# Kernel tuning notes

Measured on AMD Instinct MI355X. Metric: run time of the kernel, lower is better.

Reference implementation:

```python
import jax, jax.numpy as jnp
import numpy as np

H = 16  # heads
EPS_LN = 1e-5

def _ln(x, g, b):
    m = jnp.mean(x, axis=-1, keepdims=True)
    v = jnp.mean((x - m) ** 2, axis=-1, keepdims=True)
    return (x - m) / jnp.sqrt(v + EPS_LN) * g + b

def setup_inputs() -> dict:
    key = jax.random.key(0)
    B, L, d, mlp = 4, 4096, 1024, 4096
    ks = jax.random.split(key, 12)
    s = 0.02
    inp = {
        'x':   jax.random.normal(ks[0], (B, L, d), jnp.float32),
        'Wq':  jax.random.normal(ks[1], (d, d), jnp.float32) * s,
        'bq':  jnp.zeros((d,), jnp.float32),
        'gq':  jnp.ones((d,), jnp.float32),
        'betaq': jnp.zeros((d,), jnp.float32),
        'Wk':  jax.random.normal(ks[2], (d, d), jnp.float32) * s,
        'bk':  jnp.zeros((d,), jnp.float32),
        'gk':  jnp.ones((d,), jnp.float32),
        'betak': jnp.zeros((d,), jnp.float32),
        'Wv':  jax.random.normal(ks[3], (d, d), jnp.float32) * s,
        'bv':  jnp.zeros((d,), jnp.float32),
        'gv':  jnp.ones((d,), jnp.float32),
        'betav': jnp.zeros((d,), jnp.float32),
        'Wfq': jax.random.normal(ks[4], (d, d), jnp.float32) * s,
        'bfq': jnp.zeros((d,), jnp.float32),
        'Wfk': jax.random.normal(ks[5], (d, d), jnp.float32) * s,
        'bfk': jnp.zeros((d,), jnp.float32),
        'ga':  jnp.ones((d,), jnp.float32),
        'ba':  jnp.zeros((d,), jnp.float32),
        'W1':  jax.random.normal(ks[6], (d, mlp), jnp.float32) * s,
        'b1':  jnp.zeros((mlp,), jnp.float32),
        'W2':  jax.random.normal(ks[7], (mlp, d), jnp.float32) * s,
        'b2':  jnp.zeros((d,), jnp.float32),
    }
    return inp

def _fwd(x, Wq, bq, gq, betaq, Wk, bk, gk, betak, Wv, bv, gv, betav,
         Wfq, bfq, Wfk, bfk, ga, ba, W1, b1, W2, b2):
    B, L, d = x.shape
    D = d // H
    # Q/K/V projections + LayerNorm (dropout is eval-mode identity)
    Q = _ln(x @ Wq + bq, gq, betaq)                      # [B,L,d]
    Kc = _ln(x @ Wk + bk, gk, betak)                     # [B,L,d]
    Vc = _ln(x @ Wv + bv, gv, betav)                     # [B,L,d]
    # prepend zero token to K and V (add_zero_token=True)
    z = jnp.zeros((B, 1, d), x.dtype)
    K = jnp.concatenate([z, Kc], axis=1)                 # [B,Lk,d], Lk=L+1
    V = jnp.concatenate([z, Vc], axis=1)
    # kernel feature maps: tanh(Linear(.)) + 1
    phi_Q = jnp.tanh(Q @ Wfq + bfq) + 1.0
    phi_K = jnp.tanh(K @ Wfk + bfk) + 1.0
    split = lambda t: t.reshape(B, t.shape[1], H, D).transpose(0, 2, 1, 3)
    Qh, Kh, Vh = split(Q), split(K), split(V)            # [B,H,L(,k),D]
    pQ, pK = split(phi_Q), split(phi_K)
    # probe-softmax gating of phi_K
    q_probe = jnp.mean(Qh, axis=2) / jnp.sqrt(jnp.asarray(D, x.dtype))  # [B,H,D]
    score = jax.nn.softmax(jnp.einsum('bhd,bhkd->bhk', q_probe, Kh), axis=-1)  # [B,H,Lk]
    pKw = pK * score[..., None]                          # [B,H,Lk,D]
    # linear-attention fast path
    KV = jnp.einsum('bhkd,bhke->bhde', pKw, Vh)          # [B,H,D,D]
    Ksum = jnp.sum(pKw, axis=2)                          # [B,H,D]
    num = jnp.einsum('bhqd,bhde->bhqe', pQ, KV)          # [B,H,L,D]
    den = jnp.einsum('bhqd,bhd->bhq', pQ, Ksum)[..., None] + 1e-6
    out = num / den                                      # [B,H,L,D]
    out = out.transpose(0, 2, 1, 3).reshape(B, L, d)     # merge heads
    a = _ln(out, ga, ba)                                 # attn_norm
    # Residual MLP: a + Linear2(GELU(Linear1(a)))  (exact erf GELU)
    h = a + (jax.nn.gelu(a @ W1 + b1, approximate=False) @ W2 + b2)
    return h + x                                         # outer residual

def reference(x, Wq, bq, gq, betaq, Wk, bk, gk, betak, Wv, bv, gv, betav,
              Wfq, bfq, Wfk, bfk, ga, ba, W1, b1, W2, b2):
    return _fwd(x, Wq, bq, gq, betaq, Wk, bk, gk, betak, Wv, bv, gv, betav,
                Wfq, bfq, Wfk, bfk, ga, ba, W1, b1, W2, b2)
```

## Files before the change

kernel.cpp:

```cpp
#include <hip/hip_runtime.h>
#include <cstddef>
#include <cstdint>

static constexpr int Bc   = 4;
static constexpr int Lq   = 4096;
static constexpr int Dm   = 1024;
static constexpr int Dmlp = 4096;
static constexpr int Mrows = Bc * Lq;
static constexpr int Lk1   = Lq + 1;

typedef unsigned short u16;
typedef __bf16 bf16_t;
typedef bf16_t bf16x8 __attribute__((ext_vector_type(8)));
typedef float  f32x4  __attribute__((ext_vector_type(4)));

__device__ __forceinline__ u16 f2b(float f) {
    uint32_t u = __builtin_bit_cast(uint32_t, f);
    return (u16)((u + 0x7FFFu + ((u >> 16) & 1u)) >> 16);
}
__device__ __forceinline__ float b2f(u16 h) {
    uint32_t u = ((uint32_t)h) << 16;
    return __builtin_bit_cast(float, u);
}

#define GLL16(gsrc, ldst) \
    __builtin_amdgcn_global_load_lds( \
        (const __attribute__((address_space(1))) void*)(gsrc), \
        (__attribute__((address_space(3))) void*)(ldst), 16, 0, 0)

__global__ __launch_bounds__(256)
void zero_kernel(float* __restrict__ p, int n) {
    const int i = blockIdx.x * 256 + threadIdx.x;
    if (i < n) p[i] = 0.0f;
}

__global__ __launch_bounds__(256)
void cvt_bf16_kernel(const float* __restrict__ in, u16* __restrict__ outp, int n) {
    for (int i = (blockIdx.x * 256 + threadIdx.x) * 4; i < n; i += gridDim.x * 256 * 4) {
        float4 v = *(const float4*)&in[i];
        ushort4 o = { f2b(v.x), f2b(v.y), f2b(v.z), f2b(v.w) };
        *(ushort4*)&outp[i] = o;
    }
}

__global__ __launch_bounds__(256)
void transpose_bf16_kernel(const float* __restrict__ in, u16* __restrict__ outp,
                           int R, int C) {
    __shared__ float tile[64][65];
    const int r0 = blockIdx.y * 64, c0 = blockIdx.x * 64;
    const int t = threadIdx.x;
    const int lr = t >> 2, lc0 = (t & 3) * 16;
    #pragma unroll
    for (int j = 0; j < 4; ++j) {
        float4 v = *(const float4*)&in[(size_t)(r0 + lr) * C + c0 + lc0 + j * 4];
        tile[lr][lc0 + j * 4 + 0] = v.x;
        tile[lr][lc0 + j * 4 + 1] = v.y;
        tile[lr][lc0 + j * 4 + 2] = v.z;
        tile[lr][lc0 + j * 4 + 3] = v.w;
    }
    __syncthreads();
    const int oc = t >> 2, rr0 = (t & 3) * 16;
    union { u16 u[16]; uint4 v[2]; } pk;
    #pragma unroll
    for (int j = 0; j < 16; ++j) pk.u[j] = f2b(tile[rr0 + j][oc]);
    u16* po = &outp[(size_t)(c0 + oc) * R + r0 + rr0];
    *(uint4*)&po[0] = pk.v[0];
    *(uint4*)&po[8] = pk.v[1];
}

__global__ __launch_bounds__(256)
void kvt_cvt_kernel(const float* __restrict__ KV, u16* __restrict__ KVT) {
    const int bh = blockIdx.x;
    __shared__ float t[64][65];
    const int tid = threadIdx.x;
    const int r = tid >> 2, c0 = (tid & 3) * 16;
    const float* src = &KV[(size_t)bh * 4096];
    #pragma unroll
    for (int j = 0; j < 4; ++j) {
        float4 v = *(const float4*)&src[r * 64 + c0 + j * 4];
        t[r][c0 + j * 4 + 0] = v.x;
        t[r][c0 + j * 4 + 1] = v.y;
        t[r][c0 + j * 4 + 2] = v.z;
        t[r][c0 + j * 4 + 3] = v.w;
    }
    __syncthreads();
    const int e = tid >> 2, d0 = (tid & 3) * 16;
    union { u16 u[16]; uint4 v[2]; } pk;
    #pragma unroll
    for (int j = 0; j < 16; ++j) pk.u[j] = f2b(t[d0 + j][e]);
    u16* po = &KVT[(size_t)bh * 4096 + e * 64 + d0];
    *(uint4*)&po[0] = pk.v[0];
    *(uint4*)&po[8] = pk.v[1];
}

template<int ACT, bool RES, bool ACCUM, bool BIAS, bool OBF16>
__global__ __launch_bounds__(512, 1)
void mfma_gemm256(const u16* __restrict__ A, int ldA,
                  const u16* __restrict__ Bt, int ldB,
                  const float* __restrict__ bias,
                  void* __restrict__ Cout,
                  const u16* __restrict__ res1, const float* __restrict__ res2,
                  int M, int N, int K) {
    __shared__ u16 ldsA[4][8192];
    __shared__ u16 ldsB[4][8192];
    const int tid = threadIdx.x;
    const int l   = tid & 63;
    const int w   = tid >> 6;
    const int wm  = w >> 2;
    const int wn  = w & 3;
    const int l16 = l & 15, l4 = l >> 4;

    const int gx = N >> 8;
    int bid = blockIdx.x;
    bid = (bid & 7) * ((int)gridDim.x >> 3) + (bid >> 3);
    const int brow = (bid / gx) << 8;
    const int bcol = (bid % gx) << 8;

    const int srow = w * 16 + (l >> 2);
    const int skof = ((l & 3) ^ ((l >> 3) & 3)) << 3;
    const u16* gA = A  + (size_t)(brow + srow) * ldA + skof;
    const u16* gB = Bt + (size_t)(bcol + srow) * ldB + skof;
    const size_t gsA = (size_t)128 * ldA;
    const size_t gsB = (size_t)128 * ldB;
    const int ldst = w * 512 + l * 8;

    const int koff_rd = ((l4 ^ ((l16 >> 1) & 3)) << 3);
    const int aRdBase = (wm * 128 + l16) * 32 + koff_rd;
    const int bRdBase = (wn * 64  + l16) * 32 + koff_rd;

    f32x4 acc[8][4];
    const f32x4 zf = {0.f, 0.f, 0.f, 0.f};
    #pragma unroll
    for (int m = 0; m < 8; ++m)
        #pragma unroll
        for (int n = 0; n < 4; ++n) acc[m][n] = zf;

    auto stageA = [&](int slot, int kelem) {
        const u16* s = gA + (size_t)kelem;
        GLL16(s,       &ldsA[slot][ldst]);
        GLL16(s + gsA, &ldsA[slot][ldst + 4096]);
    };
    auto stageB = [&](int slot, int kelem) {
        const u16* s = gB + (size_t)kelem;
        GLL16(s,       &ldsB[slot][ldst]);
        GLL16(s + gsB, &ldsB[slot][ldst + 4096]);
    };

    const int T = K >> 5;
    stageA(0, 0);  stageB(0, 0);
    stageA(1, 32); stageB(1, 32);
    stageA(2, 64); stageB(2, 64);

    auto step = [&](int t, int waitsel, bool do_stage) {
        asm volatile("s_waitcnt lgkmcnt(0)" ::: "memory");
        if (waitsel == 0)      asm volatile("s_waitcnt vmcnt(8)" ::: "memory");
        else if (waitsel == 1) asm volatile("s_waitcnt vmcnt(4)" ::: "memory");
        else                   asm volatile("s_waitcnt vmcnt(0)" ::: "memory");
        asm volatile("s_barrier" ::: "memory");
        const int slot = t & 3;
        bf16x8 afr[4], bfr[4];
        #pragma unroll
        for (int n = 0; n < 4; ++n)
            bfr[n] = *(const bf16x8*)&ldsB[slot][bRdBase + n * 512];
        #pragma unroll
        for (int m = 0; m < 4; ++m)
            afr[m] = *(const bf16x8*)&ldsA[slot][aRdBase + m * 512];
        if (do_stage) stageA((t + 3) & 3, (t + 3) * 32);
        __builtin_amdgcn_s_setprio(1);
        #pragma unroll
        for (int m = 0; m < 4; ++m)
            #pragma unroll
            for (int n = 0; n < 4; ++n)
                acc[m][n] = __builtin_amdgcn_mfma_f32_16x16x32_bf16(
                    afr[m], bfr[n], acc[m][n], 0, 0, 0);
        __builtin_amdgcn_s_setprio(0);
        #pragma unroll
        for (int m = 0; m < 4; ++m)
            afr[m] = *(const bf16x8*)&ldsA[slot][aRdBase + (m + 4) * 512];
        if (do_stage) stageB((t + 3) & 3, (t + 3) * 32);
        __builtin_amdgcn_s_setprio(1);
        #pragma unroll
        for (int m = 0; m < 4; ++m)
            #pragma unroll
            for (int n = 0; n < 4; ++n)
                acc[m + 4][n] = __builtin_amdgcn_mfma_f32_16x16x32_bf16(
                    afr[m], bfr[n], acc[m + 4][n], 0, 0, 0);
        __builtin_amdgcn_s_setprio(0);
    };

    for (int t = 0; t < T - 2; ++t) step(t, 0, (t + 3) < T);
    step(T - 2, 1, false);
    step(T - 1, 2, false);

    float bvn[4];
    int coln[4];
    #pragma unroll
    for (int n = 0; n < 4; ++n) {
        coln[n] = bcol + wn * 64 + n * 16 + l16;
        bvn[n] = BIAS ? bias[coln[n]] : 0.f;
    }
    #pragma unroll
    for (int m = 0; m < 8; ++m) {
        #pragma unroll
        for (int q = 0; q < 4; ++q) {
            const size_t row = (size_t)brow + wm * 128 + m * 16 + l4 * 4 + q;
            #pragma unroll
            for (int n = 0; n < 4; ++n) {
                float v = acc[m][n][q] + bvn[n];
                if (ACT == 1) v = tanhf(v) + 1.0f;
                if (ACT == 2) v = 0.5f * v * (1.0f + erff(v * 0.70710678118654752f));
                const size_t idx = row * (size_t)N + coln[n];
                if (OBF16) {
                    ((u16*)Cout)[idx] = f2b(v);
                } else {
                    float* Cf = (float*)Cout;
                    if (ACCUM) v += Cf[idx];
                    if (RES)   v += b2f(res1[idx]) + res2[idx];
                    Cf[idx] = v;
                }
            }
        }
    }
}

__global__ __launch_bounds__(256)
void ln1024_bf16_kernel(const u16* __restrict__ in, u16* __restrict__ outp,
                        const float* __restrict__ g, const float* __restrict__ be) {
    const size_t base = (size_t)blockIdx.x * Dm;
    const int tid = threadIdx.x;
    ushort4 raw = *(const ushort4*)&in[base + tid * 4];
    float v0 = b2f(raw.x), v1 = b2f(raw.y), v2 = b2f(raw.z), v3 = b2f(raw.w);
    float s  = v0 + v1 + v2 + v3;
    float sq = v0 * v0 + v1 * v1 + v2 * v2 + v3 * v3;
    #pragma unroll
    for (int off = 32; off > 0; off >>= 1) {
        s  += __shfl_down(s,  off, 64);
        sq += __shfl_down(sq, off, 64);
    }
    __shared__ float rs[4], rq[4];
    const int lane = tid & 63, wv = tid >> 6;
    if (lane == 0) { rs[wv] = s; rq[wv] = sq; }
    __syncthreads();
    s  = rs[0] + rs[1] + rs[2] + rs[3];
    sq = rq[0] + rq[1] + rq[2] + rq[3];
    const float mean = s * (1.0f / 1024.0f);
    const float var  = sq * (1.0f / 1024.0f) - mean * mean;
    const float inv  = rsqrtf(var + 1e-5f);
    float4 gv = *(const float4*)&g[tid * 4];
    float4 bv = *(const float4*)&be[tid * 4];
    ushort4 o;
    o.x = f2b((v0 - mean) * inv * gv.x + bv.x);
    o.y = f2b((v1 - mean) * inv * gv.y + bv.y);
    o.z = f2b((v2 - mean) * inv * gv.z + bv.z);
    o.w = f2b((v3 - mean) * inv * gv.w + bv.w);
    *(ushort4*)&outp[base + tid * 4] = o;
}

__global__ __launch_bounds__(256)
void qprobe_kernel(const u16* __restrict__ Q, float* __restrict__ qp) {
    const int b = blockIdx.z;
    const int col = blockIdx.x * 256 + threadIdx.x;
    const int lchunk = Lq / 16;
    const int l0 = blockIdx.y * lchunk;
    const u16* p = Q + ((size_t)b * Lq + l0) * Dm + col;
    float s = 0.f;
    for (int l = 0; l < lchunk; ++l, p += Dm) s += b2f(*p);
    atomicAdd(&qp[b * Dm + col], s * (1.0f / (4096.0f * 8.0f)));
}

__global__ __launch_bounds__(256)
void logits_kernel(const u16* __restrict__ Kc, const float* __restrict__ qp,
                   float* __restrict__ score) {
    const int bh = blockIdx.y, b = bh >> 4, h = bh & 15;
    __shared__ float q[64];
    if (threadIdx.x < 64) q[threadIdx.x] = qp[b * Dm + h * 64 + threadIdx.x];
    __syncthreads();
    const int kr = blockIdx.x * 256 + threadIdx.x;
    const ushort4* krp = (const ushort4*)&Kc[((size_t)b * Lq + kr) * Dm + h * 64];
    float s = 0.f;
    #pragma unroll
    for (int i = 0; i < 16; ++i) {
        ushort4 v = krp[i];
        s += q[i * 4 + 0] * b2f(v.x) + q[i * 4 + 1] * b2f(v.y)
           + q[i * 4 + 2] * b2f(v.z) + q[i * 4 + 3] * b2f(v.w);
    }
    score[(size_t)bh * Lk1 + kr + 1] = s;
    if (blockIdx.x == 0 && threadIdx.x == 0) score[(size_t)bh * Lk1] = 0.f;
}

__global__ __launch_bounds__(256)
void softmax4097_kernel(float* __restrict__ sc) {
    __shared__ float buf[Lk1];
    __shared__ float red[8];
    const size_t base = (size_t)blockIdx.x * Lk1;
    const int tid = threadIdx.x;
    float mx = -1e30f;
    for (int i = tid; i < Lk1; i += 256) { float v = sc[base + i]; buf[i] = v; mx = fmaxf(mx, v); }
    #pragma unroll
    for (int off = 32; off > 0; off >>= 1) mx = fmaxf(mx, __shfl_down(mx, off, 64));
    const int lane = tid & 63, wv = tid >> 6;
    if (lane == 0) red[wv] = mx;
    __syncthreads();
    mx = fmaxf(fmaxf(red[0], red[1]), fmaxf(red[2], red[3]));
    float sum = 0.f;
    for (int i = tid; i < Lk1; i += 256) { float e = expf(buf[i] - mx); buf[i] = e; sum += e; }
    #pragma unroll
    for (int off = 32; off > 0; off >>= 1) sum += __shfl_down(sum, off, 64);
    if (lane == 0) red[4 + wv] = sum;
    __syncthreads();
    sum = red[4] + red[5] + red[6] + red[7];
    const float inv = 1.0f / sum;
    for (int i = tid; i < Lk1; i += 256) sc[base + i] = buf[i] * inv;
}

__global__ __launch_bounds__(256)
void kv_kernel(const u16* __restrict__ phiK, const u16* __restrict__ Vc,
               const float* __restrict__ sc, float* __restrict__ KV) {
    const int bh = blockIdx.y, b = bh >> 4, h = bh & 15;
    const int lchunk = Lq / 8;
    const int l0 = blockIdx.x * lchunk;
    __shared__ float pk[8][64];
    __shared__ float vv[8][64];
    const int i0 = (threadIdx.x >> 4) << 2;
    const int j0 = (threadIdx.x & 15) << 2;
    float acc[4][4] = {};
    for (int lb = l0; lb < l0 + lchunk; lb += 8) {
        #pragma unroll
        for (int q = 0; q < 2; ++q) {
            const int idx = threadIdx.x + q * 256;
            const int r = idx >> 6, c = idx & 63;
            const float scv = sc[(size_t)bh * Lk1 + lb + r + 1];
            const size_t off = ((size_t)b * Lq + lb + r) * Dm + h * 64 + c;
            pk[r][c] = b2f(phiK[off]) * scv;
            vv[r][c] = b2f(Vc[off]);
        }
        __syncthreads();
        #pragma unroll
        for (int r = 0; r < 8; ++r) {
            float ra[4], rb[4];
            #pragma unroll
            for (int i = 0; i < 4; ++i) ra[i] = pk[r][i0 + i];
            #pragma unroll
            for (int j = 0; j < 4; ++j) rb[j] = vv[r][j0 + j];
            #pragma unroll
            for (int i = 0; i < 4; ++i)
                #pragma unroll
                for (int j = 0; j < 4; ++j)
                    acc[i][j] = fmaf(ra[i], rb[j], acc[i][j]);
        }
        __syncthreads();
    }
    #pragma unroll
    for (int i = 0; i < 4; ++i)
        #pragma unroll
        for (int j = 0; j < 4; ++j)
            atomicAdd(&KV[((size_t)bh * 64 + i0 + i) * 64 + j0 + j], acc[i][j]);
}

__global__ __launch_bounds__(64)
void ksum_kernel(const u16* __restrict__ phiK, const float* __restrict__ sc,
                 const float* __restrict__ bfk, float* __restrict__ Ksum) {
    const int bh = blockIdx.y, b = bh >> 4, h = bh & 15;
    const int lchunk = Lq / 8;
    const int l0 = blockIdx.x * lchunk;
    const int dd = threadIdx.x;
    float s = 0.f;
    const u16* pp = &phiK[((size_t)b * Lq + l0) * Dm + h * 64 + dd];
    const float* sp = &sc[(size_t)bh * Lk1 + l0 + 1];
    for (int l = 0; l < lchunk; ++l, pp += Dm) s = fmaf(b2f(*pp), sp[l], s);
    if (blockIdx.x == 0) s += sc[(size_t)bh * Lk1] * (tanhf(bfk[h * 64 + dd]) + 1.0f);
    atomicAdd(&Ksum[bh * 64 + dd], s);
}

__global__ __launch_bounds__(256, 2)
void attnout_mfma_kernel(const u16* __restrict__ phiQ, const u16* __restrict__ KVT,
                         const float* __restrict__ Ksum, u16* __restrict__ outp) {
    __shared__ u16 pqs[256 * 64];
    __shared__ float kss[64];
    __shared__ float dns[256];
    const int bh = blockIdx.y, b = bh >> 4, h = bh & 15;
    const int l0 = blockIdx.x * 256;
    const int tid = threadIdx.x;
    const int l = tid & 63, w = tid >> 6;
    const int l16 = l & 15, l4 = l >> 4;

    bf16x8 bfr[4][2];
    {
        const u16* kb = KVT + (size_t)bh * 4096;
        #pragma unroll
        for (int n = 0; n < 4; ++n)
            #pragma unroll
            for (int kk = 0; kk < 2; ++kk)
                bfr[n][kk] = *(const bf16x8*)&kb[(n * 16 + l16) * 64 + kk * 32 + l4 * 8];
    }
    if (tid < 64) kss[tid] = Ksum[bh * 64 + tid];

    {
        const int rsub = tid >> 3;
        const int ssrc = ((tid & 7) ^ (rsub & 7)) * 8;
        u16* ldst = &pqs[(size_t)tid * 8];
        #pragma unroll
        for (int j = 0; j < 8; ++j) {
            const u16* g = phiQ + (((size_t)(b * Lq + l0 + j * 32 + rsub)) << 10)
                          + h * 64 + ssrc;
            GLL16(g, ldst + j * 2048);
        }
    }
    __syncthreads();

    {
        const int r7 = tid & 7;
        float s = 0.f;
        #pragma unroll
        for (int sl = 0; sl < 8; ++sl) {
            bf16x8 v = *(const bf16x8*)&pqs[tid * 64 + ((sl ^ r7) << 3)];
            #pragma unroll
            for (int j = 0; j < 8; ++j) s = fmaf(b2f(((u16*)&v)[j]), kss[sl * 8 + j], s);
        }
        dns[tid] = 1.0f / (s + 1e-6f);
    }

    f32x4 acc[4][4];
    const f32x4 zf = {0.f, 0.f, 0.f, 0.f};
    #pragma unroll
    for (int m = 0; m < 4; ++m)
        #pragma unroll
        for (int n = 0; n < 4; ++n) acc[m][n] = zf;
    #pragma unroll
    for (int kk = 0; kk < 2; ++kk) {
        bf16x8 afr[4];
        #pragma unroll
        for (int m = 0; m < 4; ++m) {
            const int row = w * 64 + m * 16 + l16;
            afr[m] = *(const bf16x8*)&pqs[row * 64 + (((kk * 4 + l4) ^ (row & 7)) << 3)];
        }
        #pragma unroll
        for (int m = 0; m < 4; ++m)
            #pragma unroll
            for (int n = 0; n < 4; ++n)
                acc[m][n] = __builtin_amdgcn_mfma_f32_16x16x32_bf16(
                    afr[m], bfr[n][kk], acc[m][n], 0, 0, 0);
    }
    __syncthreads();

    #pragma unroll
    for (int m = 0; m < 4; ++m) {
        #pragma unroll
        for (int q = 0; q < 4; ++q) {
            const int rl = w * 64 + m * 16 + l4 * 4 + q;
            const float dn = dns[rl];
            const size_t rowg = ((size_t)(b * Lq + l0 + rl)) << 10;
            #pragma unroll
            for (int n = 0; n < 4; ++n)
                outp[rowg + h * 64 + n * 16 + l16] = f2b(acc[m][n][q] * dn);
        }
    }
}

extern "C" void kernel_launch(void* const* d_in, const int* in_sizes, int n_in,
                              void* d_out, int out_size, void* d_ws, size_t ws_size,
                              hipStream_t stream) {
    const float* x     = (const float*)d_in[0];
    const float* Wq    = (const float*)d_in[1];
    const float* bq    = (const float*)d_in[2];
    const float* gq    = (const float*)d_in[3];
    const float* betaq = (const float*)d_in[4];
    const float* Wk    = (const float*)d_in[5];
    const float* bk    = (const float*)d_in[6];
    const float* gk    = (const float*)d_in[7];
    const float* betak = (const float*)d_in[8];
    const float* Wv    = (const float*)d_in[9];
    const float* bv    = (const float*)d_in[10];
    const float* gv    = (const float*)d_in[11];
    const float* betav = (const float*)d_in[12];
    const float* Wfq   = (const float*)d_in[13];
    const float* bfq   = (const float*)d_in[14];
    const float* Wfk   = (const float*)d_in[15];
    const float* bfk   = (const float*)d_in[16];
    const float* ga    = (const float*)d_in[17];
    const float* ba    = (const float*)d_in[18];
    const float* W1    = (const float*)d_in[19];
    const float* b1    = (const float*)d_in[20];
    const float* W2    = (const float*)d_in[21];
    const float* b2    = (const float*)d_in[22];
    float* outp = (float*)d_out;

    uint8_t* wsb = (uint8_t*)d_ws;
    size_t off = 0;
    auto alloc = [&](size_t bytes) { void* p = wsb + off; off += bytes; return p; };
    const size_t Md = (size_t)Mrows * Dm;
    u16* B0   = (u16*)alloc(Md * 2);
    u16* B1   = (u16*)alloc(Md * 2);
    u16* B2   = (u16*)alloc(Md * 2);
    u16* Wtq  = (u16*)alloc((size_t)Dm * Dm * 2);
    u16* Wtk  = (u16*)alloc((size_t)Dm * Dm * 2);
    u16* Wtv  = (u16*)alloc((size_t)Dm * Dm * 2);
    u16* Wtfq = (u16*)alloc((size_t)Dm * Dm * 2);
    u16* Wtfk = (u16*)alloc((size_t)Dm * Dm * 2);
    u16* Wt1  = (u16*)alloc((size_t)Dm * Dmlp * 2);
    u16* Wt2  = (u16*)alloc((size_t)Dm * Dmlp * 2);
    float* qp    = (float*)alloc(4096 * 4);
    float* KV    = (float*)alloc((size_t)64 * 64 * 64 * 4);
    float* Ksum  = (float*)alloc(4096 * 4);
    float* score = (float*)alloc((size_t)64 * Lk1 * 4);
    u16* KVT     = (u16*)alloc((size_t)64 * 64 * 64 * 2);
    u16* PK = (u16*)outp;
    u16* PQ = (u16*)outp + Md;

    const dim3 blk(256);
    const dim3 blk512(512);
    const dim3 gA(256);
    const dim3 gM(512);

    cvt_bf16_kernel<<<2048, blk, 0, stream>>>(x, B0, (int)Md);
    transpose_bf16_kernel<<<dim3(16, 16), blk, 0, stream>>>(Wq,  Wtq,  Dm, Dm);
    transpose_bf16_kernel<<<dim3(16, 16), blk, 0, stream>>>(Wk,  Wtk,  Dm, Dm);
    transpose_bf16_kernel<<<dim3(16, 16), blk, 0, stream>>>(Wv,  Wtv,  Dm, Dm);
    transpose_bf16_kernel<<<dim3(16, 16), blk, 0, stream>>>(Wfq, Wtfq, Dm, Dm);
    transpose_bf16_kernel<<<dim3(16, 16), blk, 0, stream>>>(Wfk, Wtfk, Dm, Dm);
    transpose_bf16_kernel<<<dim3(64, 16), blk, 0, stream>>>(W1,  Wt1,  Dm, Dmlp);
    transpose_bf16_kernel<<<dim3(16, 64), blk, 0, stream>>>(W2,  Wt2,  Dmlp, Dm);
    {
        const int nz = 4096 + 64 * 64 * 64 + 4096;
        zero_kernel<<<(nz + 255) / 256, blk, 0, stream>>>(qp, nz);
    }

    mfma_gemm256<0, false, false, true, true><<<gA, blk512, 0, stream>>>(
        B0, Dm, Wtq, Dm, bq, B1, nullptr, nullptr, Mrows, Dm, Dm);
    ln1024_bf16_kernel<<<Mrows, blk, 0, stream>>>(B1, B1, gq, betaq);
    mfma_gemm256<0, false, false, true, true><<<gA, blk512, 0, stream>>>(
        B0, Dm, Wtk, Dm, bk, B2, nullptr, nullptr, Mrows, Dm, Dm);
    ln1024_bf16_kernel<<<Mrows, blk, 0, stream>>>(B2, B2, gk, betak);

    qprobe_kernel<<<dim3(Dm / 256, 16, Bc), blk, 0, stream>>>(B1, qp);
    logits_kernel<<<dim3(Lq / 256, 64), blk, 0, stream>>>(B2, qp, score);
    softmax4097_kernel<<<64, blk, 0, stream>>>(score);

    mfma_gemm256<1, false, false, true, true><<<gA, blk512, 0, stream>>>(
        B2, Dm, Wtfk, Dm, bfk, PK, nullptr, nullptr, Mrows, Dm, Dm);
    mfma_gemm256<1, false, false, true, true><<<gA, blk512, 0, stream>>>(
        B1, Dm, Wtfq, Dm, bfq, PQ, nullptr, nullptr, Mrows, Dm, Dm);

    mfma_gemm256<0, false, false, true, true><<<gA, blk512, 0, stream>>>(
        B0, Dm, Wtv, Dm, bv, B1, nullptr, nullptr, Mrows, Dm, Dm);
    ln1024_bf16_kernel<<<Mrows, blk, 0, stream>>>(B1, B1, gv, betav);

    kv_kernel<<<dim3(8, 64), blk, 0, stream>>>(PK, B1, score, KV);
    ksum_kernel<<<dim3(8, 64), dim3(64), 0, stream>>>(PK, score, bfk, Ksum);
    kvt_cvt_kernel<<<64, blk, 0, stream>>>(KV, KVT);

    attnout_mfma_kernel<<<dim3(Lq / 256, 64), blk, 0, stream>>>(PQ, KVT, Ksum, B2);
    ln1024_bf16_kernel<<<Mrows, blk, 0, stream>>>(B2, B2, ga, ba);

    u16* H1 = B0;
    for (int c = 0; c < 2; ++c) {
        mfma_gemm256<2, false, false, true, true><<<gM, blk512, 0, stream>>>(
            B2, Dm, Wt1 + (size_t)c * 2048 * Dm, Dm, b1 + c * 2048,
            H1, nullptr, nullptr, Mrows, 2048, Dm);
        if (c == 0) {
            mfma_gemm256<0, false, false, true, false><<<gA, blk512, 0, stream>>>(
                H1, 2048, Wt2 + (size_t)c * 2048, Dmlp, b2,
                outp, nullptr, nullptr, Mrows, Dm, 2048);
        } else {
            mfma_gemm256<0, true, true, false, false><<<gA, blk512, 0, stream>>>(
                H1, 2048, Wt2 + (size_t)c * 2048, Dmlp, nullptr,
                outp, B2, x, Mrows, Dm, 2048);
        }
    }
}
```

Measured before the change: 782.5 us.

## Restructure GEMM main loop into 64-wide K tiles with phased barrier pipeline

Rewrites the bf16 MFMA GEMM mainloop to use 64-element K tiles double-buffered as two 32-wide halves, with a new LDS layout and XOR swizzle. Global-to-LDS loads are issued as fine-grained pieces interleaved between four MFMA phases per tile, separated by explicit barriers, sched_barrier and priority raising. The aim is better overlap of memory loads with MFMA work and fewer LDS bank conflicts. The cost is more barriers per K step, and the new swizzle indexing must be correct.

```diff
diff --git a/kernel.cpp b/kernel.cpp
--- a/kernel.cpp
+++ b/kernel.cpp
@@ -92,6 +92,16 @@
     *(uint4*)&po[0] = pk.v[0];
     *(uint4*)&po[8] = pk.v[1];
 }
+
+#define PH_SYNC() do { __builtin_amdgcn_s_barrier(); \
+    asm volatile("s_waitcnt lgkmcnt(0)" ::: "memory"); \
+    __builtin_amdgcn_sched_barrier(0); \
+    __builtin_amdgcn_s_setprio(1); } while (0)
+#define PH_END(wc) do { __builtin_amdgcn_s_setprio(0); \
+    if ((wc) == 8) asm volatile("s_waitcnt vmcnt(8)" ::: "memory"); \
+    else if ((wc) == 4) asm volatile("s_waitcnt vmcnt(4)" ::: "memory"); \
+    else if ((wc) == 0) asm volatile("s_waitcnt vmcnt(0)" ::: "memory"); \
+    __builtin_amdgcn_s_barrier(); } while (0)
 
 template<int ACT, bool RES, bool ACCUM, bool BIAS, bool OBF16>
 __global__ __launch_bounds__(512, 1)
@@ -101,8 +111,8 @@
                   void* __restrict__ Cout,
                   const u16* __restrict__ res1, const float* __restrict__ res2,
                   int M, int N, int K) {
-    __shared__ u16 ldsA[4][8192];
-    __shared__ u16 ldsB[4][8192];
+    __shared__ u16 ldsA[32768];
+    __shared__ u16 ldsB[32768];
     const int tid = threadIdx.x;
     const int l   = tid & 63;
     const int w   = tid >> 6;
@@ -116,17 +126,16 @@
     const int brow = (bid / gx) << 8;
     const int bcol = (bid % gx) << 8;
 
-    const int srow = w * 16 + (l >> 2);
-    const int skof = ((l & 3) ^ ((l >> 3) & 3)) << 3;
-    const u16* gA = A  + (size_t)(brow + srow) * ldA + skof;
-    const u16* gB = Bt + (size_t)(bcol + srow) * ldB + skof;
-    const size_t gsA = (size_t)128 * ldA;
-    const size_t gsB = (size_t)128 * ldB;
-    const int ldst = w * 512 + l * 8;
-
-    const int koff_rd = ((l4 ^ ((l16 >> 1) & 3)) << 3);
-    const int aRdBase = (wm * 128 + l16) * 32 + koff_rd;
-    const int bRdBase = (wn * 64  + l16) * 32 + koff_rd;
+    const int logi  = (tid & 7) ^ ((tid >> 3) & 7);
+    const int srow0 = 2 * (tid >> 3) + (logi >> 2);
+    const int skel  = (logi & 3) << 3;
+    u16* sdstA = ldsA + tid * 8;
+    u16* sdstB = ldsB + tid * 8;
+
+    const int lline = l16 >> 1;
+    const int physd = (l4 + ((l16 & 1) << 2)) ^ lline;
+    const int aBase = (wm * 64 + lline) * 64 + physd * 8;
+    const int bBase = (wn * 32 + lline) * 64 + physd * 8;
 
     f32x4 acc[8][4];
     const f32x4 zf = {0.f, 0.f, 0.f, 0.f};
@@ -135,62 +144,92 @@
         #pragma unroll
         for (int n = 0; n < 4; ++n) acc[m][n] = zf;
 
-    auto stageA = [&](int slot, int kelem) {
-        const u16* s = gA + (size_t)kelem;
-        GLL16(s,       &ldsA[slot][ldst]);
-        GLL16(s + gsA, &ldsA[slot][ldst + 4096]);
+    const int T_ = K >> 6;
+    const int PMAX = 4 * T_;
+
+    auto stage_piece = [&](int idx) {
+        const int isB = idx & 1, kh = (idx >> 1) & 1, tau = idx >> 2;
+        const int kof = tau * 64 + kh * 32 + skel;
+        const int lof = (((tau & 1) << 1) | kh) * 8192;
+        if (!isB) {
+            const u16* g = A + (size_t)(brow + srow0) * ldA + kof;
+            GLL16(g, sdstA + lof);
+            GLL16(g + (size_t)128 * ldA, sdstA + lof + 4096);
+        } else {
+            const u16* g = Bt + (size_t)(bcol + srow0) * ldB + kof;
+            GLL16(g, sdstB + lof);
+            GLL16(g + (size_t)128 * ldB, sdstB + lof + 4096);
+        }
     };
-    auto stageB = [&](int slot, int kelem) {
-        const u16* s = gB + (size_t)kelem;
-        GLL16(s,       &ldsB[slot][ldst]);
-        GLL16(s + gsB, &ldsB[slot][ldst + 4096]);
-    };
-
-    const int T = K >> 5;
-    stageA(0, 0);  stageB(0, 0);
-    stageA(1, 32); stageB(1, 32);
-    stageA(2, 64); stageB(2, 64);
-
-    auto step = [&](int t, int waitsel, bool do_stage) {
-        asm volatile("s_waitcnt lgkmcnt(0)" ::: "memory");
-        if (waitsel == 0)      asm volatile("s_waitcnt vmcnt(8)" ::: "memory");
-        else if (waitsel == 1) asm volatile("s_waitcnt vmcnt(4)" ::: "memory");
-        else                   asm volatile("s_waitcnt vmcnt(0)" ::: "memory");
-        asm volatile("s_barrier" ::: "memory");
-        const int slot = t & 3;
+
+    auto do_tile = [&](int t, int buf, int w1, int w3) {
+        const u16* A0 = ldsA + (buf * 2 + 0) * 8192;
+        const u16* A1 = ldsA + (buf * 2 + 1) * 8192;
+        const u16* B0 = ldsB + (buf * 2 + 0) * 8192;
+        const u16* B1 = ldsB + (buf * 2 + 1) * 8192;
+        const int base = 4 * t;
         bf16x8 afr[4], bfr[4];
         #pragma unroll
-        for (int n = 0; n < 4; ++n)
-            bfr[n] = *(const bf16x8*)&ldsB[slot][bRdBase + n * 512];
-        #pragma unroll
-        for (int m = 0; m < 4; ++m)
-            afr[m] = *(const bf16x8*)&ldsA[slot][aRdBase + m * 512];
-        if (do_stage) stageA((t + 3) & 3, (t + 3) * 32);
-        __builtin_amdgcn_s_setprio(1);
+        for (int n = 0; n < 4; ++n) bfr[n] = *(const bf16x8*)&B0[bBase + n * 512];
+        #pragma unroll
+        for (int m = 0; m < 4; ++m) afr[m] = *(const bf16x8*)&A0[aBase + m * 512];
+        if (base + 6 < PMAX) stage_piece(base + 6);
+        PH_SYNC();
         #pragma unroll
         for (int m = 0; m < 4; ++m)
             #pragma unroll
             for (int n = 0; n < 4; ++n)
                 acc[m][n] = __builtin_amdgcn_mfma_f32_16x16x32_bf16(
                     afr[m], bfr[n], acc[m][n], 0, 0, 0);
-        __builtin_amdgcn_s_setprio(0);
-        #pragma unroll
-        for (int m = 0; m < 4; ++m)
-            afr[m] = *(const bf16x8*)&ldsA[slot][aRdBase + (m + 4) * 512];
-        if (do_stage) stageB((t + 3) & 3, (t + 3) * 32);
-        __builtin_amdgcn_s_setprio(1);
+        PH_END(-1);
+        #pragma unroll
+        for (int m = 0; m < 4; ++m) afr[m] = *(const bf16x8*)&A0[aBase + (m + 4) * 512];
+        if (base + 7 < PMAX) stage_piece(base + 7);
+        PH_SYNC();
         #pragma unroll
         for (int m = 0; m < 4; ++m)
             #pragma unroll
             for (int n = 0; n < 4; ++n)
                 acc[m + 4][n] = __builtin_amdgcn_mfma_f32_16x16x32_bf16(
                     afr[m], bfr[n], acc[m + 4][n], 0, 0, 0);
-        __builtin_amdgcn_s_setprio(0);
+        PH_END(w1);
+        #pragma unroll
+        for (int n = 0; n < 4; ++n) bfr[n] = *(const bf16x8*)&B1[bBase + n * 512];
+        #pragma unroll
+        for (int m = 0; m < 4; ++m) afr[m] = *(const bf16x8*)&A1[aBase + m * 512];
+        if (base + 8 < PMAX) stage_piece(base + 8);
+        PH_SYNC();
+        #pragma unroll
+        for (int m = 0; m < 4; ++m)
+            #pragma unroll
+            for (int n = 0; n < 4; ++n)
+                acc[m][n] = __builtin_amdgcn_mfma_f32_16x16x32_bf16(
+                    afr[m], bfr[n], acc[m][n], 0, 0, 0);
+        PH_END(-1);
+        #pragma unroll
+        for (int m = 0; m < 4; ++m) afr[m] = *(const bf16x8*)&A1[aBase + (m + 4) * 512];
+        if (base + 9 < PMAX) stage_piece(base + 9);
+        PH_SYNC();
+        #pragma unroll
+        for (int m = 0; m < 4; ++m)
+            #pragma unroll
+            for (int n = 0; n < 4; ++n)
+                acc[m + 4][n] = __builtin_amdgcn_mfma_f32_16x16x32_bf16(
+                    afr[m], bfr[n], acc[m + 4][n], 0, 0, 0);
+        PH_END(w3);
     };
 
-    for (int t = 0; t < T - 2; ++t) step(t, 0, (t + 3) < T);
-    step(T - 2, 1, false);
-    step(T - 1, 2, false);
+    #pragma unroll
+    for (int i = 0; i < 6; ++i) stage_piece(i);
+    asm volatile("s_waitcnt vmcnt(8)" ::: "memory");
+    __builtin_amdgcn_s_barrier();
+
+    for (int t = 0; t < T_ - 2; t += 2) {
+        do_tile(t, 0, 8, 8);
+        do_tile(t + 1, 1, 8, 8);
+    }
+    do_tile(T_ - 2, 0, 8, 4);
+    do_tile(T_ - 1, 1, 0, -1);
 
     float bvn[4];
     int coln[4];
```

Measured after the change: 799.8 us. 1.02x slower.

## Software-pipeline LDS fragment loads one k-step ahead in GEMM main loop

Applied to the files above, without the earlier changes.

Restructures the GEMM main loop so the A/B register fragments for the next k-slice are read from LDS while the current slice's MFMAs run (register double-buffering). Both global-to-LDS stages for slice t+3 are now issued together at the top of each step. The per-step lgkmcnt(0) wait goes away, leaving a single wait-and-barrier per step with adjusted vmcnt thresholds. The intent is to hide LDS read latency behind MFMA work, at the cost of roughly 32 extra VGPRs for the prefetched fragments, which could lower occupancy or cause spills.

```diff
diff --git a/kernel.cpp b/kernel.cpp
--- a/kernel.cpp
+++ b/kernel.cpp
@@ -150,47 +150,57 @@
     stageA(0, 0);  stageB(0, 0);
     stageA(1, 32); stageB(1, 32);
     stageA(2, 64); stageB(2, 64);
-
-    auto step = [&](int t, int waitsel, bool do_stage) {
-        asm volatile("s_waitcnt lgkmcnt(0)" ::: "memory");
-        if (waitsel == 0)      asm volatile("s_waitcnt vmcnt(8)" ::: "memory");
-        else if (waitsel == 1) asm volatile("s_waitcnt vmcnt(4)" ::: "memory");
-        else                   asm volatile("s_waitcnt vmcnt(0)" ::: "memory");
-        asm volatile("s_barrier" ::: "memory");
+    asm volatile("s_waitcnt vmcnt(8)" ::: "memory");
+    __builtin_amdgcn_s_barrier();
+
+    bf16x8 a0[4], b0[4];
+    #pragma unroll
+    for (int n = 0; n < 4; ++n) b0[n] = *(const bf16x8*)&ldsB[0][bRdBase + n * 512];
+    #pragma unroll
+    for (int m = 0; m < 4; ++m) a0[m] = *(const bf16x8*)&ldsA[0][aRdBase + m * 512];
+
+    for (int t = 0; t < T; ++t) {
+        if (t == T - 2)     asm volatile("s_waitcnt vmcnt(0)" ::: "memory");
+        else if (t < T - 2) asm volatile("s_waitcnt vmcnt(4)" ::: "memory");
+        __builtin_amdgcn_s_barrier();
         const int slot = t & 3;
-        bf16x8 afr[4], bfr[4];
-        #pragma unroll
-        for (int n = 0; n < 4; ++n)
-            bfr[n] = *(const bf16x8*)&ldsB[slot][bRdBase + n * 512];
+        if (t + 3 < T) { stageA((t + 3) & 3, (t + 3) * 32); stageB((t + 3) & 3, (t + 3) * 32); }
+        bf16x8 a1[4];
         #pragma unroll
         for (int m = 0; m < 4; ++m)
-            afr[m] = *(const bf16x8*)&ldsA[slot][aRdBase + m * 512];
-        if (do_stage) stageA((t + 3) & 3, (t + 3) * 32);
+            a1[m] = *(const bf16x8*)&ldsA[slot][aRdBase + (m + 4) * 512];
+        bf16x8 an[4], bn[4];
+        if (t + 1 < T) {
+            const int ns = (t + 1) & 3;
+            #pragma unroll
+            for (int n = 0; n < 4; ++n) bn[n] = *(const bf16x8*)&ldsB[ns][bRdBase + n * 512];
+            #pragma unroll
+            for (int m = 0; m < 4; ++m) an[m] = *(const bf16x8*)&ldsA[ns][aRdBase + m * 512];
+        } else {
+            #pragma unroll
+            for (int n = 0; n < 4; ++n) bn[n] = b0[n];
+            #pragma unroll
+            for (int m = 0; m < 4; ++m) an[m] = a0[m];
+        }
         __builtin_amdgcn_s_setprio(1);
         #pragma unroll
         for (int m = 0; m < 4; ++m)
             #pragma unroll
             for (int n = 0; n < 4; ++n)
                 acc[m][n] = __builtin_amdgcn_mfma_f32_16x16x32_bf16(
-                    afr[m], bfr[n], acc[m][n], 0, 0, 0);
-        __builtin_amdgcn_s_setprio(0);
-        #pragma unroll
-        for (int m = 0; m < 4; ++m)
-            afr[m] = *(const bf16x8*)&ldsA[slot][aRdBase + (m + 4) * 512];
-        if (do_stage) stageB((t + 3) & 3, (t + 3) * 32);
-        __builtin_amdgcn_s_setprio(1);
+                    a0[m], b0[n], acc[m][n], 0, 0, 0);
         #pragma unroll
         for (int m = 0; m < 4; ++m)
             #pragma unroll
             for (int n = 0; n < 4; ++n)
                 acc[m + 4][n] = __builtin_amdgcn_mfma_f32_16x16x32_bf16(
-                    afr[m], bfr[n], acc[m + 4][n], 0, 0, 0);
+                    a1[m], b0[n], acc[m + 4][n], 0, 0, 0);
         __builtin_amdgcn_s_setprio(0);
-    };
-
-    for (int t = 0; t < T - 2; ++t) step(t, 0, (t + 3) < T);
-    step(T - 2, 1, false);
-    step(T - 1, 2, false);
+        #pragma unroll
+        for (int m = 0; m < 4; ++m) a0[m] = an[m];
+        #pragma unroll
+        for (int n = 0; n < 4; ++n) b0[n] = bn[n];
+    }
 
     float bvn[4];
     int coln[4];
```

After: 941.3 us. +20.3%, slower.

## Replace pipelined 256x256 GEMM with simple 256x128 single-buffer tile at two blocks per CU

Applied to the files above, without the earlier changes.

Rewrites the MFMA GEMM to use 256x128 tiles with 256 threads and a single LDS buffer per operand, dropping the 4-slot software pipeline, manual waitcnt scheduling and priority hints. Grids double to cover the smaller tiles, and launch bounds allow two blocks per CU. The goal is to hide memory latency through occupancy instead of explicit prefetch. In exchange, each K-step now waits for its own global loads behind two barriers, and B-tile reuse per block is halved.

```diff
diff --git a/kernel.cpp b/kernel.cpp
--- a/kernel.cpp
+++ b/kernel.cpp
@@ -94,35 +94,36 @@
 }
 
 template<int ACT, bool RES, bool ACCUM, bool BIAS, bool OBF16>
-__global__ __launch_bounds__(512, 1)
+__global__ __launch_bounds__(256, 2)
 void mfma_gemm256(const u16* __restrict__ A, int ldA,
                   const u16* __restrict__ Bt, int ldB,
                   const float* __restrict__ bias,
                   void* __restrict__ Cout,
                   const u16* __restrict__ res1, const float* __restrict__ res2,
                   int M, int N, int K) {
-    __shared__ u16 ldsA[4][8192];
-    __shared__ u16 ldsB[4][8192];
+    __shared__ u16 As[8192];
+    __shared__ u16 Bs[4096];
     const int tid = threadIdx.x;
     const int l   = tid & 63;
     const int w   = tid >> 6;
-    const int wm  = w >> 2;
-    const int wn  = w & 3;
+    const int wm  = w >> 1;
+    const int wn  = w & 1;
     const int l16 = l & 15, l4 = l >> 4;
 
-    const int gx = N >> 8;
+    const int gx = N >> 7;
     int bid = blockIdx.x;
     bid = (bid & 7) * ((int)gridDim.x >> 3) + (bid >> 3);
     const int brow = (bid / gx) << 8;
-    const int bcol = (bid % gx) << 8;
-
-    const int srow = w * 16 + (l >> 2);
-    const int skof = ((l & 3) ^ ((l >> 3) & 3)) << 3;
+    const int bcol = (bid % gx) << 7;
+
+    const int srow = tid >> 2;
+    const int skof = ((tid & 3) ^ ((tid >> 3) & 3)) << 3;
     const u16* gA = A  + (size_t)(brow + srow) * ldA + skof;
     const u16* gB = Bt + (size_t)(bcol + srow) * ldB + skof;
-    const size_t gsA = (size_t)128 * ldA;
-    const size_t gsB = (size_t)128 * ldB;
-    const int ldst = w * 512 + l * 8;
+    const size_t gsA = (size_t)64 * ldA;
+    const size_t gsB = (size_t)64 * ldB;
+    u16* lA = As + tid * 8;
+    u16* lB = Bs + tid * 8;
 
     const int koff_rd = ((l4 ^ ((l16 >> 1) & 3)) << 3);
     const int aRdBase = (wm * 128 + l16) * 32 + koff_rd;
@@ -135,62 +136,31 @@
         #pragma unroll
         for (int n = 0; n < 4; ++n) acc[m][n] = zf;
 
-    auto stageA = [&](int slot, int kelem) {
-        const u16* s = gA + (size_t)kelem;
-        GLL16(s,       &ldsA[slot][ldst]);
-        GLL16(s + gsA, &ldsA[slot][ldst + 4096]);
-    };
-    auto stageB = [&](int slot, int kelem) {
-        const u16* s = gB + (size_t)kelem;
-        GLL16(s,       &ldsB[slot][ldst]);
-        GLL16(s + gsB, &ldsB[slot][ldst + 4096]);
-    };
-
     const int T = K >> 5;
-    stageA(0, 0);  stageB(0, 0);
-    stageA(1, 32); stageB(1, 32);
-    stageA(2, 64); stageB(2, 64);
-
-    auto step = [&](int t, int waitsel, bool do_stage) {
-        asm volatile("s_waitcnt lgkmcnt(0)" ::: "memory");
-        if (waitsel == 0)      asm volatile("s_waitcnt vmcnt(8)" ::: "memory");
-        else if (waitsel == 1) asm volatile("s_waitcnt vmcnt(4)" ::: "memory");
-        else                   asm volatile("s_waitcnt vmcnt(0)" ::: "memory");
-        asm volatile("s_barrier" ::: "memory");
-        const int slot = t & 3;
-        bf16x8 afr[4], bfr[4];
+    for (int t = 0; t < T; ++t) {
+        GLL16(gA,           lA);
+        GLL16(gA +     gsA, lA + 2048);
+        GLL16(gA + 2 * gsA, lA + 4096);
+        GLL16(gA + 3 * gsA, lA + 6144);
+        GLL16(gB,           lB);
+        GLL16(gB +     gsB, lB + 2048);
+        gA += 32; gB += 32;
+        __syncthreads();
+        bf16x8 bfr[4], afr[8];
         #pragma unroll
         for (int n = 0; n < 4; ++n)
-            bfr[n] = *(const bf16x8*)&ldsB[slot][bRdBase + n * 512];
-        #pragma unroll
-        for (int m = 0; m < 4; ++m)
-            afr[m] = *(const bf16x8*)&ldsA[slot][aRdBase + m * 512];
-        if (do_stage) stageA((t + 3) & 3, (t + 3) * 32);
-        __builtin_amdgcn_s_setprio(1);
-        #pragma unroll
-        for (int m = 0; m < 4; ++m)
+            bfr[n] = *(const bf16x8*)&Bs[bRdBase + n * 512];
+        #pragma unroll
+        for (int m = 0; m < 8; ++m)
+            afr[m] = *(const bf16x8*)&As[aRdBase + m * 512];
+        #pragma unroll
+        for (int m = 0; m < 8; ++m)
             #pragma unroll
             for (int n = 0; n < 4; ++n)
                 acc[m][n] = __builtin_amdgcn_mfma_f32_16x16x32_bf16(
                     afr[m], bfr[n], acc[m][n], 0, 0, 0);
-        __builtin_amdgcn_s_setprio(0);
-        #pragma unroll
-        for (int m = 0; m < 4; ++m)
-            afr[m] = *(const bf16x8*)&ldsA[slot][aRdBase + (m + 4) * 512];
-        if (do_stage) stageB((t + 3) & 3, (t + 3) * 32);
-        __builtin_amdgcn_s_setprio(1);
-        #pragma unroll
-        for (int m = 0; m < 4; ++m)
-            #pragma unroll
-            for (int n = 0; n < 4; ++n)
-                acc[m + 4][n] = __builtin_amdgcn_mfma_f32_16x16x32_bf16(
-                    afr[m], bfr[n], acc[m + 4][n], 0, 0, 0);
-        __builtin_amdgcn_s_setprio(0);
-    };
-
-    for (int t = 0; t < T - 2; ++t) step(t, 0, (t + 3) < T);
-    step(T - 2, 1, false);
-    step(T - 1, 2, false);
+        __syncthreads();
+    }
 
     float bvn[4];
     int coln[4];
@@ -508,9 +478,8 @@
     u16* PQ = (u16*)outp + Md;
 
     const dim3 blk(256);
-    const dim3 blk512(512);
-    const dim3 gA(256);
-    const dim3 gM(512);
+    const dim3 gP(512);
+    const dim3 gM1(1024);
 
     cvt_bf16_kernel<<<2048, blk, 0, stream>>>(x, B0, (int)Md);
     transpose_bf16_kernel<<<dim3(16, 16), blk, 0, stream>>>(Wq,  Wtq,  Dm, Dm);
@@ -525,10 +494,10 @@
         zero_kernel<<<(nz + 255) / 256, blk, 0, stream>>>(qp, nz);
     }
 
-    mfma_gemm256<0, false, false, true, true><<<gA, blk512, 0, stream>>>(
+    mfma_gemm256<0, false, false, true, true><<<gP, blk, 0, stream>>>(
         B0, Dm, Wtq, Dm, bq, B1, nullptr, nullptr, Mrows, Dm, Dm);
     ln1024_bf16_kernel<<<Mrows, blk, 0, stream>>>(B1, B1, gq, betaq);
-    mfma_gemm256<0, false, false, true, true><<<gA, blk512, 0, stream>>>(
+    mfma_gemm256<0, false, false, true, true><<<gP, blk, 0, stream>>>(
         B0, Dm, Wtk, Dm, bk, B2, nullptr, nullptr, Mrows, Dm, Dm);
     ln1024_bf16_kernel<<<Mrows, blk, 0, stream>>>(B2, B2, gk, betak);
 
@@ -536,12 +505,12 @@
     logits_kernel<<<dim3(Lq / 256, 64), blk, 0, stream>>>(B2, qp, score);
     softmax4097_kernel<<<64, blk, 0, stream>>>(score);
 
-    mfma_gemm256<1, false, false, true, true><<<gA, blk512, 0, stream>>>(
+    mfma_gemm256<1, false, false, true, true><<<gP, blk, 0, stream>>>(
         B2, Dm, Wtfk, Dm, bfk, PK, nullptr, nullptr, Mrows, Dm, Dm);
-    mfma_gemm256<1, false, false, true, true><<<gA, blk512, 0, stream>>>(
+    mfma_gemm256<1, false, false, true, true><<<gP, blk, 0, stream>>>(
         B1, Dm, Wtfq, Dm, bfq, PQ, nullptr, nullptr, Mrows, Dm, Dm);
 
-    mfma_gemm256<0, false, false, true, true><<<gA, blk512, 0, stream>>>(
+    mfma_gemm256<0, false, false, true, true><<<gP, blk, 0, stream>>>(
         B0, Dm, Wtv, Dm, bv, B1, nullptr, nullptr, Mrows, Dm, Dm);
     ln1024_bf16_kernel<<<Mrows, blk, 0, stream>>>(B1, B1, gv, betav);
 
@@ -554,15 +523,15 @@
 
     u16* H1 = B0;
     for (int c = 0; c < 2; ++c) {
-        mfma_gemm256<2, false, false, true, true><<<gM, blk512, 0, stream>>>(
+        mfma_gemm256<2, false, false, true, true><<<gM1, blk, 0, stream>>>(
             B2, Dm, Wt1 + (size_t)c * 2048 * Dm, Dm, b1 + c * 2048,
             H1, nullptr, nullptr, Mrows, 2048, Dm);
         if (c == 0) {
-            mfma_gemm256<0, false, false, true, false><<<gA, blk512, 0, stream>>>(
+            mfma_gemm256<0, false, false, true, false><<<gP, blk, 0, stream>>>(
                 H1, 2048, Wt2 + (size_t)c * 2048, Dmlp, b2,
                 outp, nullptr, nullptr, Mrows, Dm, 2048);
         } else {
-            mfma_gemm256<0, true, true, false, false><<<gA, blk512, 0, stream>>>(
+            mfma_gemm256<0, true, true, false, false><<<gP, blk, 0, stream>>>(
                 H1, 2048, Wt2 + (size_t)c * 2048, Dmlp, nullptr,
                 outp, B2, x, Mrows, Dm, 2048);
         }
```

Measured after the change: 850.5 us. 1.09x slower.
